# Performance work log

Hardware: AMD Instinct MI355X
Metric: run time of the kernel (lower is better)

Reference implementation:

```python
import jax, jax.numpy as jnp
import numpy as np

B, L, A, HD, H = 4096, 512, 64, 1024, 32
EPS = 1e-5


def _ln(x, g, b):
    m = jnp.mean(x, axis=-1, keepdims=True)
    v = jnp.mean((x - m) ** 2, axis=-1, keepdims=True)
    return (x - m) * jax.lax.rsqrt(v + EPS) * g + b


def setup_inputs() -> dict:
    key = jax.random.key(0)
    ks = jax.random.split(key, 12)
    s = 0.02
    return {
        "z_0": jax.random.normal(ks[0], (B, L), jnp.float32),
        "actions": jax.random.normal(ks[1], (B, H, A), jnp.float32),
        "W1": jax.random.normal(ks[2], (L + A, HD), jnp.float32) * s,
        "b1": jnp.zeros((HD,), jnp.float32),
        "g1": jnp.ones((HD,), jnp.float32),
        "be1": jnp.zeros((HD,), jnp.float32),
        "W2": jax.random.normal(ks[3], (HD, HD), jnp.float32) * s,
        "b2": jnp.zeros((HD,), jnp.float32),
        "g2": jnp.ones((HD,), jnp.float32),
        "be2": jnp.zeros((HD,), jnp.float32),
        "W3": jax.random.normal(ks[4], (HD, L), jnp.float32) * s,
        "b3": jnp.zeros((L,), jnp.float32),
        "uW1": jax.random.normal(ks[5], (L, HD // 2), jnp.float32) * s,
        "ub1": jnp.zeros((HD // 2,), jnp.float32),
        "uW2": jax.random.normal(ks[6], (HD // 2, 1), jnp.float32) * s,
        "ub2": jnp.zeros((1,), jnp.float32),
        "gate": jnp.asarray(0.5, jnp.float32),
    }


def reference(z_0, actions, W1, b1, g1, be1, W2, b2, g2, be2, W3, b3,
              uW1, ub1, uW2, ub2, gate):
    gate_s = jax.nn.sigmoid(gate)

    def step_fn(z, a):
        za = jnp.concatenate([z, a], axis=-1)              # [B, L+A]
        h = jax.nn.gelu(_ln(za @ W1 + b1, g1, be1), approximate=False)
        h = jax.nn.gelu(_ln(h @ W2 + b2, g2, be2), approximate=False)
        dz = h @ W3 + b3                                   # [B, L]
        z_next = z + gate_s * dz
        u = jax.nn.gelu(z_next @ uW1 + ub1, approximate=False)
        sigma = jax.nn.softplus(u @ uW2 + ub2)             # [B, 1]
        return z_next, (z_next, sigma)

    a_seq = jnp.swapaxes(actions, 0, 1)                    # [H, B, A]
    _, (traj, sigs) = jax.lax.scan(step_fn, z_0, a_seq)
    return jnp.swapaxes(traj, 0, 1), jnp.swapaxes(sigs, 0, 1)
```

## Files before the change

### kernel.cpp

```cpp
#include <hip/hip_runtime.h>
#include <hip/hip_bf16.h>
#include <math.h>

#define B_SZ 4096
#define L_SZ 512
#define A_SZ 64
#define HD_SZ 1024
#define H_SZ 32

typedef __attribute__((ext_vector_type(8))) short bf16x8;
typedef __attribute__((ext_vector_type(4))) short s16x4;
typedef __attribute__((ext_vector_type(4))) float f32x4;

#define GLDS16(gsrc, ldst) __builtin_amdgcn_global_load_lds(              \
    (const __attribute__((address_space(1))) void*)(gsrc),                \
    (__attribute__((address_space(3))) void*)(ldst), 16, 0, 0)

__device__ __forceinline__ float gelu_exact(float x) {
  return 0.5f * x * (1.0f + erff(x * 0.70710678118654752f));
}

template <int BM, int BN, int MODE>
__global__ __launch_bounds__(256, 2) void gemm_kernel(
    const __hip_bfloat16* __restrict__ A0, int a0s,
    const __hip_bfloat16* __restrict__ A1, int a1s, int ksplit,
    const __hip_bfloat16* __restrict__ Bt,
    const float* __restrict__ bias,
    int N, int K,
    float* __restrict__ outf,
    float* __restrict__ z_cur,
    __hip_bfloat16* __restrict__ znb,
    float* __restrict__ traj,
    const float* __restrict__ gate,
    int t,
    float* __restrict__ zu,
    const float* __restrict__ ub1v,
    const float* __restrict__ uW2,
    float* __restrict__ sig_acc) {
  constexpr int BK = 64;
  constexpr int ROWB = BK * 2;
  constexpr int FM = BM / 32, FN = BN / 32;
  constexpr int ABYTES = BM * ROWB;
  constexpr int BUFB = (BM + BN) * ROWB;
  __shared__ __align__(16) char lds[2 * BUFB];

  const int tid = threadIdx.x;
  const int m0 = blockIdx.x * BM, n0 = blockIdx.y * BN;
  const int wave = tid >> 6, lane = tid & 63;
  const int l15 = lane & 15, lg = lane >> 4;
  const int wm = wave >> 1, wn = wave & 1;
  const int NK = K / BK;

  f32x4 acc[FM][FN];
#pragma unroll
  for (int mi = 0; mi < FM; ++mi)
#pragma unroll
    for (int ni = 0; ni < FN; ++ni) acc[mi][ni] = (f32x4){0.f, 0.f, 0.f, 0.f};

  auto stage = [&](int buf, int kt) {
    char* dst = lds + buf * BUFB;
    const int k0 = kt * BK;
    const __hip_bfloat16* Aptr;
    int As, kloc;
    if (k0 < ksplit) { Aptr = A0; As = a0s; kloc = k0; }
    else             { Aptr = A1; As = a1s; kloc = k0 - ksplit; }
#pragma unroll
    for (int i = 0; i < BM / 32; ++i) {
      int off = tid * 16 + i * 4096;
      int r = off >> 7;
      int csw = (off & 127) ^ ((r & 7) << 4);
      GLDS16(Aptr + (size_t)(m0 + r) * As + kloc + (csw >> 1), dst + off);
    }
#pragma unroll
    for (int i = 0; i < BN / 32; ++i) {
      int off = tid * 16 + i * 4096;
      int r = off >> 7;
      int csw = (off & 127) ^ ((r & 7) << 4);
      GLDS16(Bt + (size_t)(n0 + r) * K + k0 + (csw >> 1), dst + ABYTES + off);
    }
  };

  const int xrow = (l15 & 7) << 4;
  const int offs0 = (lg * 16) ^ xrow;
  const int aoff = (wm * (FM * 16) + l15) * ROWB;
  const int boff = ABYTES + (wn * (FN * 16) + l15) * ROWB;

  stage(0, 0);
  asm volatile("s_waitcnt vmcnt(0)" ::: "memory");
  __syncthreads();

  int buf = 0;
  for (int kt = 0; kt < NK; ++kt) {
    if (kt + 1 < NK) stage(buf ^ 1, kt + 1);

    const char* lb = lds + buf * BUFB;
    bf16x8 a_[FM][2], b_[FN][2];
#pragma unroll
    for (int mi = 0; mi < FM; ++mi) {
      a_[mi][0] = *(const bf16x8*)(lb + aoff + mi * (16 * ROWB) + offs0);
      a_[mi][1] = *(const bf16x8*)(lb + aoff + mi * (16 * ROWB) + (offs0 ^ 64));
    }
#pragma unroll
    for (int ni = 0; ni < FN; ++ni) {
      b_[ni][0] = *(const bf16x8*)(lb + boff + ni * (16 * ROWB) + offs0);
      b_[ni][1] = *(const bf16x8*)(lb + boff + ni * (16 * ROWB) + (offs0 ^ 64));
    }
#pragma unroll
    for (int s = 0; s < 2; ++s)
#pragma unroll
      for (int mi = 0; mi < FM; ++mi)
#pragma unroll
        for (int ni = 0; ni < FN; ++ni)
          acc[mi][ni] = __builtin_amdgcn_mfma_f32_16x16x32_bf16(
              a_[mi][s], b_[ni][s], acc[mi][ni], 0, 0, 0);

    asm volatile("s_waitcnt vmcnt(0)" ::: "memory");
    __syncthreads();
    buf ^= 1;
  }

  if constexpr (MODE == 0) {
#pragma unroll
    for (int mi = 0; mi < FM; ++mi) {
#pragma unroll
      for (int ni = 0; ni < FN; ++ni) {
        int gcol = n0 + wn * (FN * 16) + ni * 16 + l15;
        float bv = bias[gcol];
#pragma unroll
        for (int r = 0; r < 4; ++r) {
          int grow = m0 + wm * (FM * 16) + mi * 16 + lg * 4 + r;
          outf[(size_t)grow * N + gcol] = acc[mi][ni][r] + bv;
        }
      }
    }
  } else {
    const float gs = 1.f / (1.f + expf(-gate[0]));
    if (n0 < L_SZ) {
#pragma unroll
      for (int mi = 0; mi < FM; ++mi) {
#pragma unroll
        for (int ni = 0; ni < FN; ++ni) {
          int gcol = n0 + wn * (FN * 16) + ni * 16 + l15;
          float bv = bias[gcol];
#pragma unroll
          for (int r = 0; r < 4; ++r) {
            int grow = m0 + wm * (FM * 16) + mi * 16 + lg * 4 + r;
            size_t zi = (size_t)grow * L_SZ + gcol;
            float zn = z_cur[zi] + gs * (acc[mi][ni][r] + bv);
            z_cur[zi] = zn;
            znb[zi] = __float2bfloat16(zn);
            traj[(size_t)grow * (H_SZ * L_SZ) + (size_t)t * L_SZ + gcol] = zn;
          }
        }
      }
    } else {
#pragma unroll
      for (int mi = 0; mi < FM; ++mi) {
        float p[4] = {0.f, 0.f, 0.f, 0.f};
#pragma unroll
        for (int ni = 0; ni < FN; ++ni) {
          int gcol = n0 + wn * (FN * 16) + ni * 16 + l15;
          int j = gcol - L_SZ;
          float bv = bias[gcol];
          float ub = ub1v[j];
          float w2 = uW2[j];
#pragma unroll
          for (int r = 0; r < 4; ++r) {
            int grow = m0 + wm * (FM * 16) + mi * 16 + lg * 4 + r;
            size_t ui = (size_t)grow * L_SZ + j;
            float zun = zu[ui] + gs * (acc[mi][ni][r] + bv);
            zu[ui] = zun;
            p[r] += gelu_exact(zun + ub) * w2;
          }
        }
#pragma unroll
        for (int o = 1; o < 16; o <<= 1) {
#pragma unroll
          for (int r = 0; r < 4; ++r) p[r] += __shfl_xor(p[r], o);
        }
        if (l15 == 0) {
          int rowb = m0 + wm * (FM * 16) + mi * 16 + lg * 4;
#pragma unroll
          for (int r = 0; r < 4; ++r)
            atomicAdd(&sig_acc[(size_t)(rowb + r) * H_SZ + t], p[r]);
        }
      }
    }
  }
}

__global__ __launch_bounds__(256) void ln_gelu_kernel(
    const float* __restrict__ x, const float* __restrict__ gam,
    const float* __restrict__ bet, __hip_bfloat16* __restrict__ out) {
  constexpr int N = HD_SZ;
  const int row = blockIdx.x;
  const int tid = threadIdx.x, lane = tid & 63, wave = tid >> 6;
  const float* xr = x + (size_t)row * N;
  f32x4 v = *(const f32x4*)(xr + tid * 4);
  float s = v[0] + v[1] + v[2] + v[3];
  float s2 = v[0] * v[0] + v[1] * v[1] + v[2] * v[2] + v[3] * v[3];
#pragma unroll
  for (int o = 32; o; o >>= 1) {
    s += __shfl_xor(s, o);
    s2 += __shfl_xor(s2, o);
  }
  __shared__ float as_[4], as2_[4];
  if (lane == 0) { as_[wave] = s; as2_[wave] = s2; }
  __syncthreads();
  s = as_[0] + as_[1] + as_[2] + as_[3];
  s2 = as2_[0] + as2_[1] + as2_[2] + as2_[3];
  float mean = s * (1.f / N);
  float var = s2 * (1.f / N) - mean * mean;
  float rstd = rsqrtf(var + 1e-5f);
  f32x4 g = *(const f32x4*)(gam + tid * 4);
  f32x4 b = *(const f32x4*)(bet + tid * 4);
  union { __hip_bfloat16 h[4]; s16x4 sv; } o;
#pragma unroll
  for (int j = 0; j < 4; ++j) {
    float y = (v[j] - mean) * rstd * g[j] + b[j];
    o.h[j] = __float2bfloat16(gelu_exact(y));
  }
  *(s16x4*)(out + (size_t)row * N + tid * 4) = o.sv;
}

__global__ void transpose_cvt(const float* __restrict__ in,
                              __hip_bfloat16* __restrict__ out, int K, int N) {
  __shared__ float tile[32][33];
  const int n0 = blockIdx.x * 32, k0 = blockIdx.y * 32;
  const int tx = threadIdx.x, ty = threadIdx.y;
#pragma unroll
  for (int i = 0; i < 32; i += 8)
    tile[ty + i][tx] = in[(size_t)(k0 + ty + i) * N + (n0 + tx)];
  __syncthreads();
#pragma unroll
  for (int i = 0; i < 32; i += 8)
    out[(size_t)(n0 + ty + i) * K + (k0 + tx)] = __float2bfloat16(tile[tx][ty + i]);
}

__global__ __launch_bounds__(256) void w34_kernel(
    const float* __restrict__ W3, const float* __restrict__ uW1,
    __hip_bfloat16* __restrict__ W3c) {
  __shared__ float tA[16][17];
  __shared__ float tB[16][17];
  const int k0 = blockIdx.x * 16, j0 = blockIdx.y * 16;
  const int tx = threadIdx.x & 15, ty = threadIdx.x >> 4;
  float acc = 0.f;
  for (int i0 = 0; i0 < L_SZ; i0 += 16) {
    tA[ty][tx] = W3[(size_t)(k0 + ty) * L_SZ + i0 + tx];
    tB[ty][tx] = uW1[(size_t)(i0 + ty) * (HD_SZ / 2) + j0 + tx];
    __syncthreads();
#pragma unroll
    for (int i = 0; i < 16; ++i) acc += tA[ty][i] * tB[i][tx];
    __syncthreads();
  }
  W3c[(size_t)(L_SZ + j0 + tx) * HD_SZ + k0 + ty] = __float2bfloat16(acc);
}

__global__ void bias3_kernel(const float* __restrict__ b3,
                             const float* __restrict__ uW1,
                             float* __restrict__ bias3c) {
  int j = blockIdx.x * 256 + threadIdx.x;
  if (j >= L_SZ) return;
  bias3c[j] = b3[j];
  float s = 0.f;
  for (int i = 0; i < L_SZ; ++i) s += b3[i] * uW1[(size_t)i * (HD_SZ / 2) + j];
  bias3c[L_SZ + j] = s;
}

__global__ void cvt_bf16_kernel(const float* __restrict__ in,
                                __hip_bfloat16* __restrict__ out, int n4) {
  int i = blockIdx.x * 256 + threadIdx.x;
  if (i >= n4) return;
  f32x4 v = ((const f32x4*)in)[i];
  union { __hip_bfloat16 h[4]; s16x4 sv; } o;
#pragma unroll
  for (int j = 0; j < 4; ++j) o.h[j] = __float2bfloat16(v[j]);
  ((s16x4*)out)[i] = o.sv;
}

__global__ void init_z_kernel(const float* __restrict__ z0,
                              float* __restrict__ z_cur,
                              __hip_bfloat16* __restrict__ znb, int n4) {
  int i = blockIdx.x * 256 + threadIdx.x;
  if (i >= n4) return;
  f32x4 v = ((const f32x4*)z0)[i];
  ((f32x4*)z_cur)[i] = v;
  union { __hip_bfloat16 h[4]; s16x4 sv; } o;
#pragma unroll
  for (int j = 0; j < 4; ++j) o.h[j] = __float2bfloat16(v[j]);
  ((s16x4*)znb)[i] = o.sv;
}

__global__ void zero_kernel(float* __restrict__ p, int n) {
  int i = blockIdx.x * 256 + threadIdx.x;
  if (i < n) p[i] = 0.f;
}

__global__ void softplus_kernel(const float* __restrict__ acc,
                                const float* __restrict__ ub2,
                                float* __restrict__ out, int n) {
  int i = blockIdx.x * 256 + threadIdx.x;
  if (i >= n) return;
  float v = acc[i] + ub2[0];
  out[i] = v > 20.f ? v : log1pf(expf(v));
}

extern "C" void kernel_launch(void* const* d_in, const int* in_sizes, int n_in,
                              void* d_out, int out_size, void* d_ws,
                              size_t ws_size, hipStream_t stream) {
  const float* z0      = (const float*)d_in[0];
  const float* actions = (const float*)d_in[1];
  const float* W1  = (const float*)d_in[2];
  const float* b1  = (const float*)d_in[3];
  const float* g1  = (const float*)d_in[4];
  const float* be1 = (const float*)d_in[5];
  const float* W2  = (const float*)d_in[6];
  const float* b2  = (const float*)d_in[7];
  const float* g2  = (const float*)d_in[8];
  const float* be2 = (const float*)d_in[9];
  const float* W3  = (const float*)d_in[10];
  const float* b3  = (const float*)d_in[11];
  const float* uW1 = (const float*)d_in[12];
  const float* ub1 = (const float*)d_in[13];
  const float* uW2 = (const float*)d_in[14];
  const float* ub2 = (const float*)d_in[15];
  const float* gate = (const float*)d_in[16];

  char* w = (char*)d_ws;
  __hip_bfloat16* W1t = (__hip_bfloat16*)w;  w += (size_t)(L_SZ + A_SZ) * HD_SZ * 2;
  __hip_bfloat16* W2t = (__hip_bfloat16*)w;  w += (size_t)HD_SZ * HD_SZ * 2;
  __hip_bfloat16* W3c = (__hip_bfloat16*)w;  w += (size_t)HD_SZ * HD_SZ * 2;
  __hip_bfloat16* uW1t = (__hip_bfloat16*)w; w += (size_t)L_SZ * (HD_SZ / 2) * 2;
  __hip_bfloat16* actb = (__hip_bfloat16*)w; w += (size_t)B_SZ * H_SZ * A_SZ * 2;
  float* z_cur = (float*)w;                  w += (size_t)B_SZ * L_SZ * 4;
  __hip_bfloat16* znb = (__hip_bfloat16*)w;  w += (size_t)B_SZ * L_SZ * 2;
  float* zu = (float*)w;                     w += (size_t)B_SZ * L_SZ * 4;
  float* tws = (float*)w;                    w += (size_t)B_SZ * HD_SZ * 4;
  __hip_bfloat16* hb = (__hip_bfloat16*)w;   w += (size_t)B_SZ * HD_SZ * 2;
  float* sig_acc = (float*)w;                w += (size_t)B_SZ * H_SZ * 4;
  float* bias3c = (float*)w;                 w += (size_t)HD_SZ * 4;
  float* zbias = (float*)w;                  w += (size_t)L_SZ * 4;

  float* trajOut = (float*)d_out;
  float* sigsOut = (float*)d_out + (size_t)B_SZ * H_SZ * L_SZ;

  dim3 tb(32, 8);
  transpose_cvt<<<dim3(HD_SZ / 32, (L_SZ + A_SZ) / 32), tb, 0, stream>>>(W1, W1t, L_SZ + A_SZ, HD_SZ);
  transpose_cvt<<<dim3(HD_SZ / 32, HD_SZ / 32), tb, 0, stream>>>(W2, W2t, HD_SZ, HD_SZ);
  transpose_cvt<<<dim3(L_SZ / 32, HD_SZ / 32), tb, 0, stream>>>(W3, W3c, HD_SZ, L_SZ);
  transpose_cvt<<<dim3((HD_SZ / 2) / 32, L_SZ / 32), tb, 0, stream>>>(uW1, uW1t, L_SZ, HD_SZ / 2);
  w34_kernel<<<dim3(HD_SZ / 16, L_SZ / 16), 256, 0, stream>>>(W3, uW1, W3c);
  bias3_kernel<<<2, 256, 0, stream>>>(b3, uW1, bias3c);

  cvt_bf16_kernel<<<(B_SZ * H_SZ * A_SZ / 4 + 255) / 256, 256, 0, stream>>>(
      actions, actb, B_SZ * H_SZ * A_SZ / 4);
  init_z_kernel<<<(B_SZ * L_SZ / 4 + 255) / 256, 256, 0, stream>>>(
      z0, z_cur, znb, B_SZ * L_SZ / 4);
  zero_kernel<<<(B_SZ * H_SZ + L_SZ + 255) / 256, 256, 0, stream>>>(
      sig_acc, B_SZ * H_SZ + L_SZ);
  zero_kernel<<<(L_SZ + 255) / 256, 256, 0, stream>>>(zbias, L_SZ);

  const int KSPLIT_NONE = 1 << 30;

  gemm_kernel<64, 128, 0><<<dim3(B_SZ / 64, L_SZ / 128), 256, 0, stream>>>(
      znb, L_SZ, nullptr, 0, KSPLIT_NONE, uW1t, zbias,
      L_SZ, L_SZ, zu, nullptr, nullptr, nullptr, nullptr, 0,
      nullptr, nullptr, nullptr, nullptr);

  for (int t = 0; t < H_SZ; ++t) {
    gemm_kernel<64, 128, 0><<<dim3(B_SZ / 64, HD_SZ / 128), 256, 0, stream>>>(
        znb, L_SZ, actb + (size_t)t * A_SZ, H_SZ * A_SZ, L_SZ, W1t, b1,
        HD_SZ, L_SZ + A_SZ, tws, nullptr, nullptr, nullptr, nullptr, 0,
        nullptr, nullptr, nullptr, nullptr);
    ln_gelu_kernel<<<B_SZ, 256, 0, stream>>>(tws, g1, be1, hb);
    gemm_kernel<64, 128, 0><<<dim3(B_SZ / 64, HD_SZ / 128), 256, 0, stream>>>(
        hb, HD_SZ, nullptr, 0, KSPLIT_NONE, W2t, b2,
        HD_SZ, HD_SZ, tws, nullptr, nullptr, nullptr, nullptr, 0,
        nullptr, nullptr, nullptr, nullptr);
    ln_gelu_kernel<<<B_SZ, 256, 0, stream>>>(tws, g2, be2, hb);
    gemm_kernel<64, 128, 4><<<dim3(B_SZ / 64, HD_SZ / 128), 256, 0, stream>>>(
        hb, HD_SZ, nullptr, 0, KSPLIT_NONE, W3c, bias3c,
        HD_SZ, HD_SZ, nullptr, z_cur, znb, trajOut, gate, t,
        zu, ub1, uW2, sig_acc);
  }
  softplus_kernel<<<(B_SZ * H_SZ + 255) / 256, 256, 0, stream>>>(
      sig_acc, ub2, sigsOut, B_SZ * H_SZ);
}
```

Measured before the change: 2.384 ms.

## Triple-buffer GEMM LDS pipeline and store pre-LayerNorm activations in bf16

The GEMM main loop moves from a double-buffered LDS scheme to a three-slot ring that prefetches two K-tiles ahead. It uses partial vmcnt waits and raw s_barrier instead of a full drain each iteration, so global-to-LDS loads overlap MFMA work. Separately, the W1 and W2 GEMM outputs feeding LayerNorm are written as bf16 instead of fp32, which halves that intermediate traffic in both the GEMM epilogue and the LN kernel. LDS use grows by 50%, which may affect occupancy under launch_bounds(256,2), and LayerNorm inputs lose precision.

```diff
diff --git a/kernel.cpp b/kernel.cpp
--- a/kernel.cpp
+++ b/kernel.cpp
@@ -15,6 +15,10 @@
 #define GLDS16(gsrc, ldst) __builtin_amdgcn_global_load_lds(              \
     (const __attribute__((address_space(1))) void*)(gsrc),                \
     (__attribute__((address_space(3))) void*)(ldst), 16, 0, 0)
+
+template <int N> __device__ __forceinline__ void vmwait() {
+  asm volatile("s_waitcnt vmcnt(%0)" :: "n"(N) : "memory");
+}
 
 __device__ __forceinline__ float gelu_exact(float x) {
   return 0.5f * x * (1.0f + erff(x * 0.70710678118654752f));
@@ -36,13 +40,15 @@
     float* __restrict__ zu,
     const float* __restrict__ ub1v,
     const float* __restrict__ uW2,
-    float* __restrict__ sig_acc) {
+    float* __restrict__ sig_acc,
+    __hip_bfloat16* __restrict__ outb) {
   constexpr int BK = 64;
   constexpr int ROWB = BK * 2;
   constexpr int FM = BM / 32, FN = BN / 32;
   constexpr int ABYTES = BM * ROWB;
   constexpr int BUFB = (BM + BN) * ROWB;
-  __shared__ __align__(16) char lds[2 * BUFB];
+  constexpr int LOADS = (BM + BN) / 32;
+  __shared__ __align__(16) char lds[3 * BUFB];
 
   const int tid = threadIdx.x;
   const int m0 = blockIdx.x * BM, n0 = blockIdx.y * BN;
@@ -57,8 +63,8 @@
 #pragma unroll
     for (int ni = 0; ni < FN; ++ni) acc[mi][ni] = (f32x4){0.f, 0.f, 0.f, 0.f};
 
-  auto stage = [&](int buf, int kt) {
-    char* dst = lds + buf * BUFB;
+  auto stage = [&](int slot, int kt) {
+    char* dst = lds + slot * BUFB;
     const int k0 = kt * BK;
     const __hip_bfloat16* Aptr;
     int As, kloc;
@@ -86,12 +92,21 @@
   const int boff = ABYTES + (wn * (FN * 16) + l15) * ROWB;
 
   stage(0, 0);
-  asm volatile("s_waitcnt vmcnt(0)" ::: "memory");
-  __syncthreads();
+  stage(1, 1);
 
   int buf = 0;
   for (int kt = 0; kt < NK; ++kt) {
-    if (kt + 1 < NK) stage(buf ^ 1, kt + 1);
+    if (kt + 2 < NK) {
+      int s2 = buf + 2; if (s2 >= 3) s2 -= 3;
+      stage(s2, kt + 2);
+      vmwait<2 * LOADS>();
+    } else if (kt + 1 < NK) {
+      vmwait<LOADS>();
+    } else {
+      vmwait<0>();
+    }
+    __builtin_amdgcn_s_barrier();
+    asm volatile("" ::: "memory");
 
     const char* lb = lds + buf * BUFB;
     bf16x8 a_[FM][2], b_[FN][2];
@@ -114,12 +129,12 @@
           acc[mi][ni] = __builtin_amdgcn_mfma_f32_16x16x32_bf16(
               a_[mi][s], b_[ni][s], acc[mi][ni], 0, 0, 0);
 
-    asm volatile("s_waitcnt vmcnt(0)" ::: "memory");
-    __syncthreads();
-    buf ^= 1;
-  }
-
-  if constexpr (MODE == 0) {
+    asm volatile("" ::: "memory");
+    __builtin_amdgcn_s_barrier();
+    buf = (buf + 1 == 3) ? 0 : buf + 1;
+  }
+
+  if constexpr (MODE == 0 || MODE == 5) {
 #pragma unroll
     for (int mi = 0; mi < FM; ++mi) {
 #pragma unroll
@@ -129,7 +144,11 @@
 #pragma unroll
         for (int r = 0; r < 4; ++r) {
           int grow = m0 + wm * (FM * 16) + mi * 16 + lg * 4 + r;
-          outf[(size_t)grow * N + gcol] = acc[mi][ni][r] + bv;
+          float v = acc[mi][ni][r] + bv;
+          if constexpr (MODE == 0)
+            outb[(size_t)grow * N + gcol] = __float2bfloat16(v);
+          else
+            outf[(size_t)grow * N + gcol] = v;
         }
       }
     }
@@ -190,13 +209,16 @@
 }
 
 __global__ __launch_bounds__(256) void ln_gelu_kernel(
-    const float* __restrict__ x, const float* __restrict__ gam,
+    const __hip_bfloat16* __restrict__ x, const float* __restrict__ gam,
     const float* __restrict__ bet, __hip_bfloat16* __restrict__ out) {
   constexpr int N = HD_SZ;
   const int row = blockIdx.x;
   const int tid = threadIdx.x, lane = tid & 63, wave = tid >> 6;
-  const float* xr = x + (size_t)row * N;
-  f32x4 v = *(const f32x4*)(xr + tid * 4);
+  union { s16x4 sv; __hip_bfloat16 h[4]; } in;
+  in.sv = *(const s16x4*)(x + (size_t)row * N + tid * 4);
+  float v[4];
+#pragma unroll
+  for (int j = 0; j < 4; ++j) v[j] = __bfloat162float(in.h[j]);
   float s = v[0] + v[1] + v[2] + v[3];
   float s2 = v[0] * v[0] + v[1] * v[1] + v[2] * v[2] + v[3] * v[3];
 #pragma unroll
@@ -335,7 +357,7 @@
   float* z_cur = (float*)w;                  w += (size_t)B_SZ * L_SZ * 4;
   __hip_bfloat16* znb = (__hip_bfloat16*)w;  w += (size_t)B_SZ * L_SZ * 2;
   float* zu = (float*)w;                     w += (size_t)B_SZ * L_SZ * 4;
-  float* tws = (float*)w;                    w += (size_t)B_SZ * HD_SZ * 4;
+  __hip_bfloat16* tws = (__hip_bfloat16*)w;  w += (size_t)B_SZ * HD_SZ * 2;
   __hip_bfloat16* hb = (__hip_bfloat16*)w;   w += (size_t)B_SZ * HD_SZ * 2;
   float* sig_acc = (float*)w;                w += (size_t)B_SZ * H_SZ * 4;
   float* bias3c = (float*)w;                 w += (size_t)HD_SZ * 4;
@@ -356,32 +378,31 @@
       actions, actb, B_SZ * H_SZ * A_SZ / 4);
   init_z_kernel<<<(B_SZ * L_SZ / 4 + 255) / 256, 256, 0, stream>>>(
       z0, z_cur, znb, B_SZ * L_SZ / 4);
-  zero_kernel<<<(B_SZ * H_SZ + L_SZ + 255) / 256, 256, 0, stream>>>(
-      sig_acc, B_SZ * H_SZ + L_SZ);
+  zero_kernel<<<(B_SZ * H_SZ + 255) / 256, 256, 0, stream>>>(sig_acc, B_SZ * H_SZ);
   zero_kernel<<<(L_SZ + 255) / 256, 256, 0, stream>>>(zbias, L_SZ);
 
   const int KSPLIT_NONE = 1 << 30;
 
-  gemm_kernel<64, 128, 0><<<dim3(B_SZ / 64, L_SZ / 128), 256, 0, stream>>>(
+  gemm_kernel<64, 128, 5><<<dim3(B_SZ / 64, L_SZ / 128), 256, 0, stream>>>(
       znb, L_SZ, nullptr, 0, KSPLIT_NONE, uW1t, zbias,
       L_SZ, L_SZ, zu, nullptr, nullptr, nullptr, nullptr, 0,
-      nullptr, nullptr, nullptr, nullptr);
+      nullptr, nullptr, nullptr, nullptr, nullptr);
 
   for (int t = 0; t < H_SZ; ++t) {
     gemm_kernel<64, 128, 0><<<dim3(B_SZ / 64, HD_SZ / 128), 256, 0, stream>>>(
         znb, L_SZ, actb + (size_t)t * A_SZ, H_SZ * A_SZ, L_SZ, W1t, b1,
-        HD_SZ, L_SZ + A_SZ, tws, nullptr, nullptr, nullptr, nullptr, 0,
-        nullptr, nullptr, nullptr, nullptr);
+        HD_SZ, L_SZ + A_SZ, nullptr, nullptr, nullptr, nullptr, nullptr, 0,
+        nullptr, nullptr, nullptr, nullptr, tws);
     ln_gelu_kernel<<<B_SZ, 256, 0, stream>>>(tws, g1, be1, hb);
     gemm_kernel<64, 128, 0><<<dim3(B_SZ / 64, HD_SZ / 128), 256, 0, stream>>>(
         hb, HD_SZ, nullptr, 0, KSPLIT_NONE, W2t, b2,
-        HD_SZ, HD_SZ, tws, nullptr, nullptr, nullptr, nullptr, 0,
-        nullptr, nullptr, nullptr, nullptr);
+        HD_SZ, HD_SZ, nullptr, nullptr, nullptr, nullptr, nullptr, 0,
+        nullptr, nullptr, nullptr, nullptr, tws);
     ln_gelu_kernel<<<B_SZ, 256, 0, stream>>>(tws, g2, be2, hb);
     gemm_kernel<64, 128, 4><<<dim3(B_SZ / 64, HD_SZ / 128), 256, 0, stream>>>(
         hb, HD_SZ, nullptr, 0, KSPLIT_NONE, W3c, bias3c,
         HD_SZ, HD_SZ, nullptr, z_cur, znb, trajOut, gate, t,
-        zu, ub1, uW2, sig_acc);
+        zu, ub1, uW2, sig_acc, nullptr);
   }
   softplus_kernel<<<(B_SZ * H_SZ + 255) / 256, 256, 0, stream>>>(
       sig_acc, ub2, sigsOut, B_SZ * H_SZ);
```

Result: faster. 2.253 ms (-5.5%).
